# Kernel tuning notes

Measured on AMD Instinct MI355X. Metric: run time of the kernel, lower is better.

## Reference

```python
import jax, jax.numpy as jnp
import numpy as np

L = 3          # num_modification_layers
MOD_SCALE = 0.01


def setup_inputs() -> dict:
    key = jax.random.key(0)
    B, E = 8192, 1024
    ks = jax.random.split(key, 12)
    sg = 1.0 / np.sqrt(E)        # GRUCell / Linear(E,.) init bound
    sh = 1.0 / np.sqrt(E // 2)   # Linear(E//2, E) init bound
    u = lambda k, shape, s: jax.random.uniform(k, shape, jnp.float32, -s, s)
    return {
        "x":    jax.random.normal(ks[0], (B, E), jnp.float32),
        # GRUCell params (PyTorch layout: gates ordered r, z, n)
        "W_ih": u(ks[1], (L, 3 * E, E), sg),
        "W_hh": u(ks[2], (L, 3 * E, E), sg),
        "b_ih": u(ks[3], (L, 3 * E), sg),
        "b_hh": u(ks[4], (L, 3 * E), sg),
        # modification network: Linear(E, E//2) -> ReLU -> Linear(E//2, E) -> Tanh
        "W1":   u(ks[5], (L, E // 2, E), sg),
        "b1":   u(ks[6], (L, E // 2), sg),
        "W2":   u(ks[7], (L, E, E // 2), sh),
        "b2":   u(ks[8], (L, E), sh),
        # modification gate: Linear(E, 1) -> Sigmoid
        "Wg":   u(ks[9], (L, 1, E), sg),
        "bg":   u(ks[10], (L, 1), sg),
    }


def reference(x, W_ih, W_hh, b_ih, b_hh, W1, b1, W2, b2, Wg, bg):
    B, E = x.shape
    h_prev = jnp.zeros((B, E), x.dtype)  # hidden states reset to zeros
    cur = x
    for l in range(L):
        # modification network (small MLP) + scalar gate
        sig = jnp.tanh(jax.nn.relu(cur @ W1[l].T + b1[l]) @ W2[l].T + b2[l])  # (B, E)
        gate = jax.nn.sigmoid(cur @ Wg[l].T + bg[l])                           # (B, 1)
        cond = jnp.mean(gate) > 0.5
        # data-dependent self-modification: weight_ih += scale * mean(sig)[None,:]
        # (row-broadcast over the 3E gate rows), predicated on-device
        wih = jnp.where(cond,
                        W_ih[l] + MOD_SCALE * jnp.mean(sig, axis=0)[None, :],
                        W_ih[l])
        # GRUCell (PyTorch semantics)
        gi = cur @ wih.T + b_ih[l]            # (B, 3E)
        gh = h_prev @ W_hh[l].T + b_hh[l]     # (B, 3E) -- h_prev is zeros
        i_r, i_z, i_n = jnp.split(gi, 3, axis=1)
        h_r, h_z, h_n = jnp.split(gh, 3, axis=1)
        r = jax.nn.sigmoid(i_r + h_r)
        z = jax.nn.sigmoid(i_z + h_z)
        n = jnp.tanh(i_n + r * h_n)
        h = (1.0 - z) * n + z * h_prev
        cur = h + sig
    return cur
```

## Files before the change

kernel.cpp:

```cpp
#include <hip/hip_runtime.h>
#include <cstdint>
#include <cstddef>


#define BSZ 8192
#define ESZ 1024

typedef _Float16 f16x8 __attribute__((ext_vector_type(8)));
typedef float    f32x4 __attribute__((ext_vector_type(4)));
typedef unsigned short u16;
typedef u16 u16x4 __attribute__((ext_vector_type(4)));

__device__ __forceinline__ u16 f2h(float f) {
    _Float16 h = (_Float16)f;
    return __builtin_bit_cast(u16, h);
}

__device__ __forceinline__ void gload16(const void* g, void* l) {
    __builtin_amdgcn_global_load_lds((const __attribute__((address_space(1))) void*)g,
                                     (__attribute__((address_space(3))) void*)l,
                                     16, 0, 0);
}

__device__ __forceinline__ float sigmoidf_(float x) {
    return 1.f / (1.f + __expf(-x));
}
__device__ __forceinline__ float tanhf_(float x) {
    float cx = fminf(fmaxf(x, -15.f), 15.f);
    float e = __expf(2.f * cx);
    return (e - 1.f) / (e + 1.f);
}

__global__ void cvt_f16_kernel(const float* __restrict__ in, u16* __restrict__ out, int n4) {
    int i = blockIdx.x * 256 + threadIdx.x;
    if (i >= n4) return;
    f32x4 v = ((const f32x4*)in)[i];
    u16x4 o;
    o.x = f2h(v.x); o.y = f2h(v.y); o.z = f2h(v.z); o.w = f2h(v.w);
    ((u16x4*)out)[i] = o;
}

__global__ void gate_kernel(const float* __restrict__ cur, const float* __restrict__ Wg,
                            const float* __restrict__ bg, const float* __restrict__ colsum,
                            float* __restrict__ gsum, float* __restrict__ sdot) {
    const int wid = threadIdx.x >> 6, lane = threadIdx.x & 63;
    const int row = blockIdx.x * 4 + wid;
    const float* cr = cur + (size_t)row * ESZ;
    float pg = 0.f, pm = 0.f;
#pragma unroll
    for (int c = 0; c < 4; c++) {
        int idx = c * 256 + lane * 4;
        f32x4 cv = *(const f32x4*)(cr + idx);
        f32x4 wv = *(const f32x4*)(Wg + idx);
        f32x4 mv = *(const f32x4*)(colsum + idx);
        pg += cv.x * wv.x + cv.y * wv.y + cv.z * wv.z + cv.w * wv.w;
        pm += cv.x * mv.x + cv.y * mv.y + cv.z * mv.z + cv.w * mv.w;
    }
#pragma unroll
    for (int s = 32; s >= 1; s >>= 1) {
        pg += __shfl_xor(pg, s);
        pm += __shfl_xor(pm, s);
    }
    __shared__ float gp[4];
    if (lane == 0) {
        gp[wid] = sigmoidf_(pg + bg[0]);
        sdot[row] = pm * (0.01f / 8192.f);
    }
    __syncthreads();
    if (threadIdx.x == 0) atomicAdd(gsum, gp[0] + gp[1] + gp[2] + gp[3]);
}

template <int ACT>
__global__ void __launch_bounds__(256, 2) gemm_act_kernel(
    const u16* __restrict__ A, const u16* __restrict__ W,
    const float* __restrict__ bias, void* __restrict__ outp,
    float* __restrict__ colsum, int N, int K) {
    __shared__ u16 lA[128 * 64];
    __shared__ u16 lB[128 * 64];
    const int t = threadIdx.x;
    const int m0 = blockIdx.y * 128, n0 = blockIdx.x * 128;
    const int wid = t >> 6, lane = t & 63;
    const int waver = wid >> 1, wavec = wid & 1;
    const int lrow = lane & 15, lk = lane >> 4;

    f32x4 acc[4][4] = {};

    for (int k0 = 0; k0 < K; k0 += 64) {
        __syncthreads();
#pragma unroll
        for (int i = 0; i < 4; i++) {
            int eo = i * 2048 + t * 8;
            int r = eo >> 6, c = eo & 63;
            gload16(A + (size_t)(m0 + r) * K + k0 + c, &lA[eo]);
            gload16(W + (size_t)(n0 + r) * K + k0 + c, &lB[eo]);
        }
        __syncthreads();
#pragma unroll
        for (int kk = 0; kk < 2; kk++) {
            f16x8 af[4], bf[4];
#pragma unroll
            for (int m = 0; m < 4; m++)
                af[m] = *(const f16x8*)&lA[(waver * 64 + m * 16 + lrow) * 64 + kk * 32 + lk * 8];
#pragma unroll
            for (int n = 0; n < 4; n++)
                bf[n] = *(const f16x8*)&lB[(wavec * 64 + n * 16 + lrow) * 64 + kk * 32 + lk * 8];
#pragma unroll
            for (int m = 0; m < 4; m++)
#pragma unroll
                for (int n = 0; n < 4; n++)
                    acc[m][n] = __builtin_amdgcn_mfma_f32_16x16x32_f16(af[m], bf[n], acc[m][n], 0, 0, 0);
        }
    }

#pragma unroll
    for (int n = 0; n < 4; n++) {
        int c = n0 + wavec * 64 + n * 16 + lrow;
        float bv = bias[c];
        float cs = 0.f;
#pragma unroll
        for (int m = 0; m < 4; m++) {
            int rbase = m0 + waver * 64 + m * 16 + lk * 4;
#pragma unroll
            for (int j = 0; j < 4; j++) {
                float v = acc[m][n][j] + bv;
                if (ACT == 0) {
                    v = v > 0.f ? v : 0.f;
                    ((u16*)outp)[(size_t)(rbase + j) * N + c] = f2h(v);
                } else {
                    float tv = tanhf_(v);
                    ((float*)outp)[(size_t)(rbase + j) * N + c] = tv;
                    cs += tv;
                }
            }
        }
        if (ACT == 1) {
            cs += __shfl_xor(cs, 16);
            cs += __shfl_xor(cs, 32);
            if (lane < 16) atomicAdd(&colsum[c], cs);
        }
    }
}

__global__ void __launch_bounds__(256, 2) gemm_gru_kernel(
    const u16* __restrict__ Ab, const u16* __restrict__ Wb,
    const float* __restrict__ bih, const float* __restrict__ bhh,
    const float* __restrict__ sig, const float* __restrict__ sdot,
    const float* __restrict__ gsum, float* __restrict__ curf_out,
    u16* __restrict__ curb_out) {
    __shared__ u16 lA[128 * 64];
    __shared__ u16 lB[3][64 * 64];
    const int t = threadIdx.x;
    const int m0 = blockIdx.y * 128, c0 = blockIdx.x * 64;
    const int wid = t >> 6, lane = t & 63;
    const int waver = wid >> 1, wavec = wid & 1;
    const int lrow = lane & 15, lk = lane >> 4;
    const int K = ESZ, E = ESZ;

    f32x4 acc[4][6] = {};

    for (int k0 = 0; k0 < K; k0 += 64) {
        __syncthreads();
#pragma unroll
        for (int i = 0; i < 4; i++) {
            int eo = i * 2048 + t * 8;
            int r = eo >> 6, c = eo & 63;
            gload16(Ab + (size_t)(m0 + r) * K + k0 + c, &lA[eo]);
        }
#pragma unroll
        for (int g = 0; g < 3; g++)
#pragma unroll
            for (int i = 0; i < 2; i++) {
                int eo = i * 2048 + t * 8;
                int r = eo >> 6, c = eo & 63;
                gload16(Wb + (size_t)(g * 1024 + c0 + r) * K + k0 + c, &lB[g][eo]);
            }
        __syncthreads();
#pragma unroll
        for (int kk = 0; kk < 2; kk++) {
            f16x8 af[4];
#pragma unroll
            for (int m = 0; m < 4; m++)
                af[m] = *(const f16x8*)&lA[(waver * 64 + m * 16 + lrow) * 64 + kk * 32 + lk * 8];
#pragma unroll
            for (int g = 0; g < 3; g++) {
#pragma unroll
                for (int n = 0; n < 2; n++) {
                    f16x8 bf = *(const f16x8*)&lB[g][(wavec * 32 + n * 16 + lrow) * 64 + kk * 32 + lk * 8];
#pragma unroll
                    for (int m = 0; m < 4; m++)
                        acc[m][g * 2 + n] =
                            __builtin_amdgcn_mfma_f32_16x16x32_f16(af[m], bf, acc[m][g * 2 + n], 0, 0, 0);
                }
            }
        }
    }

    const bool cond = (*gsum) > 4096.f;
#pragma unroll
    for (int m = 0; m < 4; m++) {
        int rbase = m0 + waver * 64 + m * 16 + lk * 4;
        float corr[4];
#pragma unroll
        for (int j = 0; j < 4; j++) corr[j] = cond ? sdot[rbase + j] : 0.f;
#pragma unroll
        for (int n = 0; n < 2; n++) {
            int c = c0 + wavec * 32 + n * 16 + lrow;
            float br = bih[c], bz = bih[E + c], bn = bih[2 * E + c];
            float hr = bhh[c], hz = bhh[E + c], hn = bhh[2 * E + c];
#pragma unroll
            for (int j = 0; j < 4; j++) {
                float ir = acc[m][0 + n][j] + br + corr[j];
                float iz = acc[m][2 + n][j] + bz + corr[j];
                float inn = acc[m][4 + n][j] + bn + corr[j];
                float r = sigmoidf_(ir + hr);
                float z = sigmoidf_(iz + hz);
                float nn = tanhf_(inn + r * hn);
                float h = (1.f - z) * nn;
                float o = h + sig[(size_t)(rbase + j) * E + c];
                curf_out[(size_t)(rbase + j) * E + c] = o;
                if (curb_out) curb_out[(size_t)(rbase + j) * E + c] = f2h(o);
            }
        }
    }
}

extern "C" void kernel_launch(void* const* d_in, const int* in_sizes, int n_in,
                              void* d_out, int out_size, void* d_ws, size_t ws_size,
                              hipStream_t stream) {
    const float* x   = (const float*)d_in[0];
    const float* Wih = (const float*)d_in[1];
    const float* bih = (const float*)d_in[3];
    const float* bhh = (const float*)d_in[4];
    const float* W1  = (const float*)d_in[5];
    const float* b1  = (const float*)d_in[6];
    const float* W2  = (const float*)d_in[7];
    const float* b2  = (const float*)d_in[8];
    const float* Wg  = (const float*)d_in[9];
    const float* bg  = (const float*)d_in[10];
    float* out = (float*)d_out;

    char* w = (char*)d_ws;
    u16* Wihb  = (u16*)w;  w += (size_t)3 * 3072 * 1024 * 2;
    u16* W1b   = (u16*)w;  w += (size_t)3 * 512 * 1024 * 2;
    u16* W2b   = (u16*)w;  w += (size_t)3 * 1024 * 512 * 2;
    u16* curbA = (u16*)w;  w += (size_t)BSZ * ESZ * 2;
    u16* curbB = (u16*)w;  w += (size_t)BSZ * ESZ * 2;
    u16* Amat  = (u16*)w;  w += (size_t)BSZ * 512 * 2;
    float* sigb   = (float*)w;  w += (size_t)BSZ * ESZ * 4;
    float* colsum = (float*)w;  w += 4096;
    float* gsum   = (float*)w;  w += 256;
    float* sdot   = (float*)w;  w += (size_t)BSZ * 4;

    {
        int n4 = 3 * 3072 * 1024 / 4;
        cvt_f16_kernel<<<dim3((n4 + 255) / 256), 256, 0, stream>>>(Wih, Wihb, n4);
        n4 = 3 * 512 * 1024 / 4;
        cvt_f16_kernel<<<dim3((n4 + 255) / 256), 256, 0, stream>>>(W1, W1b, n4);
        n4 = 3 * 1024 * 512 / 4;
        cvt_f16_kernel<<<dim3((n4 + 255) / 256), 256, 0, stream>>>(W2, W2b, n4);
        n4 = BSZ * ESZ / 4;
        cvt_f16_kernel<<<dim3((n4 + 255) / 256), 256, 0, stream>>>(x, curbA, n4);
    }

    u16* cin = curbA;
    u16* cout = curbB;
    for (int l = 0; l < 3; l++) {
        hipMemsetAsync(colsum, 0, 4096 + 4, stream);
        gemm_act_kernel<0><<<dim3(512 / 128, BSZ / 128), 256, 0, stream>>>(
            cin, W1b + (size_t)l * 512 * 1024, b1 + l * 512, Amat, nullptr, 512, 1024);
        gemm_act_kernel<1><<<dim3(1024 / 128, BSZ / 128), 256, 0, stream>>>(
            Amat, W2b + (size_t)l * 1024 * 512, b2 + l * 1024, sigb, colsum, 1024, 512);
        gate_kernel<<<dim3(BSZ / 4), 256, 0, stream>>>(
            l == 0 ? x : out, Wg + l * 1024, bg + l, colsum, gsum, sdot);
        gemm_gru_kernel<<<dim3(ESZ / 64, BSZ / 128), 256, 0, stream>>>(
            cin, Wihb + (size_t)l * 3072 * 1024, bih + l * 3072, bhh + l * 3072,
            sigb, sdot, gsum, out, (l < 2) ? cout : nullptr);
        u16* tmp = cin; cin = cout; cout = tmp;
    }
}
```

Baseline: 635.6 us.

## Swizzle LDS tiles, store sig as fp16, fuse converts, remap GRU blocks per XCD

```diff
diff --git a/kernel.cpp b/kernel.cpp
--- a/kernel.cpp
+++ b/kernel.cpp
@@ -15,6 +15,9 @@
     _Float16 h = (_Float16)f;
     return __builtin_bit_cast(u16, h);
 }
+__device__ __forceinline__ float h2f(u16 h) {
+    return (float)__builtin_bit_cast(_Float16, h);
+}
 
 __device__ __forceinline__ void gload16(const void* g, void* l) {
     __builtin_amdgcn_global_load_lds((const __attribute__((address_space(1))) void*)g,
@@ -22,6 +25,10 @@
                                      16, 0, 0);
 }
 
+__device__ __forceinline__ int swzi(int row, int chunk) {
+    return (row << 6) + (((chunk ^ row) & 7) << 3);
+}
+
 __device__ __forceinline__ float sigmoidf_(float x) {
     return 1.f / (1.f + __expf(-x));
 }
@@ -31,30 +38,50 @@
     return (e - 1.f) / (e + 1.f);
 }
 
-__global__ void cvt_f16_kernel(const float* __restrict__ in, u16* __restrict__ out, int n4) {
+#define N4_WIH (3 * 3072 * 1024 / 4)
+#define N4_W1  (3 * 512 * 1024 / 4)
+#define N4_W2  (3 * 1024 * 512 / 4)
+#define N4_X   (BSZ * ESZ / 4)
+
+__global__ void cvt_all_kernel(const float* __restrict__ Wih, const float* __restrict__ W1,
+                               const float* __restrict__ W2, const float* __restrict__ x,
+                               u16* __restrict__ oWih, u16* __restrict__ oW1,
+                               u16* __restrict__ oW2, u16* __restrict__ ox) {
     int i = blockIdx.x * 256 + threadIdx.x;
-    if (i >= n4) return;
+    const float* in;
+    u16* out;
+    if (i < N4_WIH) { in = Wih; out = oWih; }
+    else if (i < N4_WIH + N4_W1) { i -= N4_WIH; in = W1; out = oW1; }
+    else if (i < N4_WIH + N4_W1 + N4_W2) { i -= N4_WIH + N4_W1; in = W2; out = oW2; }
+    else { i -= N4_WIH + N4_W1 + N4_W2; if (i >= N4_X) return; in = x; out = ox; }
     f32x4 v = ((const f32x4*)in)[i];
     u16x4 o;
     o.x = f2h(v.x); o.y = f2h(v.y); o.z = f2h(v.z); o.w = f2h(v.w);
     ((u16x4*)out)[i] = o;
 }
 
-__global__ void gate_kernel(const float* __restrict__ cur, const float* __restrict__ Wg,
+__global__ void gate_kernel(const u16* __restrict__ cur, const float* __restrict__ Wg,
                             const float* __restrict__ bg, const float* __restrict__ colsum,
                             float* __restrict__ gsum, float* __restrict__ sdot) {
     const int wid = threadIdx.x >> 6, lane = threadIdx.x & 63;
     const int row = blockIdx.x * 4 + wid;
-    const float* cr = cur + (size_t)row * ESZ;
+    const u16* cr = cur + (size_t)row * ESZ;
     float pg = 0.f, pm = 0.f;
 #pragma unroll
-    for (int c = 0; c < 4; c++) {
-        int idx = c * 256 + lane * 4;
-        f32x4 cv = *(const f32x4*)(cr + idx);
-        f32x4 wv = *(const f32x4*)(Wg + idx);
-        f32x4 mv = *(const f32x4*)(colsum + idx);
-        pg += cv.x * wv.x + cv.y * wv.y + cv.z * wv.z + cv.w * wv.w;
-        pm += cv.x * mv.x + cv.y * mv.y + cv.z * mv.z + cv.w * mv.w;
+    for (int h = 0; h < 2; h++) {
+        int base = lane * 16 + h * 8;
+        f16x8 cv = *(const f16x8*)(cr + base);
+#pragma unroll
+        for (int q = 0; q < 2; q++) {
+            f32x4 wv = *(const f32x4*)(Wg + base + q * 4);
+            f32x4 mv = *(const f32x4*)(colsum + base + q * 4);
+#pragma unroll
+            for (int e = 0; e < 4; e++) {
+                float c = (float)cv[q * 4 + e];
+                pg += c * wv[e];
+                pm += c * mv[e];
+            }
+        }
     }
 #pragma unroll
     for (int s = 32; s >= 1; s >>= 1) {
@@ -73,7 +100,7 @@
 template <int ACT>
 __global__ void __launch_bounds__(256, 2) gemm_act_kernel(
     const u16* __restrict__ A, const u16* __restrict__ W,
-    const float* __restrict__ bias, void* __restrict__ outp,
+    const float* __restrict__ bias, u16* __restrict__ outp,
     float* __restrict__ colsum, int N, int K) {
     __shared__ u16 lA[128 * 64];
     __shared__ u16 lB[128 * 64];
@@ -90,9 +117,10 @@
 #pragma unroll
         for (int i = 0; i < 4; i++) {
             int eo = i * 2048 + t * 8;
-            int r = eo >> 6, c = eo & 63;
-            gload16(A + (size_t)(m0 + r) * K + k0 + c, &lA[eo]);
-            gload16(W + (size_t)(n0 + r) * K + k0 + c, &lB[eo]);
+            int r = eo >> 6;
+            int gc = (((eo >> 3) ^ r) & 7) << 3;
+            gload16(A + (size_t)(m0 + r) * K + k0 + gc, &lA[eo]);
+            gload16(W + (size_t)(n0 + r) * K + k0 + gc, &lB[eo]);
         }
         __syncthreads();
 #pragma unroll
@@ -100,10 +128,10 @@
             f16x8 af[4], bf[4];
 #pragma unroll
             for (int m = 0; m < 4; m++)
-                af[m] = *(const f16x8*)&lA[(waver * 64 + m * 16 + lrow) * 64 + kk * 32 + lk * 8];
+                af[m] = *(const f16x8*)&lA[swzi(waver * 64 + m * 16 + lrow, kk * 4 + lk)];
 #pragma unroll
             for (int n = 0; n < 4; n++)
-                bf[n] = *(const f16x8*)&lB[(wavec * 64 + n * 16 + lrow) * 64 + kk * 32 + lk * 8];
+                bf[n] = *(const f16x8*)&lB[swzi(wavec * 64 + n * 16 + lrow, kk * 4 + lk)];
 #pragma unroll
             for (int m = 0; m < 4; m++)
 #pragma unroll
@@ -125,10 +153,10 @@
                 float v = acc[m][n][j] + bv;
                 if (ACT == 0) {
                     v = v > 0.f ? v : 0.f;
-                    ((u16*)outp)[(size_t)(rbase + j) * N + c] = f2h(v);
+                    outp[(size_t)(rbase + j) * N + c] = f2h(v);
                 } else {
                     float tv = tanhf_(v);
-                    ((float*)outp)[(size_t)(rbase + j) * N + c] = tv;
+                    outp[(size_t)(rbase + j) * N + c] = f2h(tv);
                     cs += tv;
                 }
             }
@@ -144,13 +172,15 @@
 __global__ void __launch_bounds__(256, 2) gemm_gru_kernel(
     const u16* __restrict__ Ab, const u16* __restrict__ Wb,
     const float* __restrict__ bih, const float* __restrict__ bhh,
-    const float* __restrict__ sig, const float* __restrict__ sdot,
+    const u16* __restrict__ sig, const float* __restrict__ sdot,
     const float* __restrict__ gsum, float* __restrict__ curf_out,
     u16* __restrict__ curb_out) {
     __shared__ u16 lA[128 * 64];
     __shared__ u16 lB[3][64 * 64];
     const int t = threadIdx.x;
-    const int m0 = blockIdx.y * 128, c0 = blockIdx.x * 64;
+    const int hw = blockIdx.y * 16 + blockIdx.x;
+    const int xcd = hw & 7, idx = hw >> 3;
+    const int m0 = (idx >> 1) * 128, c0 = ((xcd << 1) | (idx & 1)) * 64;
     const int wid = t >> 6, lane = t & 63;
     const int waver = wid >> 1, wavec = wid & 1;
     const int lrow = lane & 15, lk = lane >> 4;
@@ -163,16 +193,18 @@
 #pragma unroll
         for (int i = 0; i < 4; i++) {
             int eo = i * 2048 + t * 8;
-            int r = eo >> 6, c = eo & 63;
-            gload16(Ab + (size_t)(m0 + r) * K + k0 + c, &lA[eo]);
+            int r = eo >> 6;
+            int gc = (((eo >> 3) ^ r) & 7) << 3;
+            gload16(Ab + (size_t)(m0 + r) * K + k0 + gc, &lA[eo]);
         }
 #pragma unroll
         for (int g = 0; g < 3; g++)
 #pragma unroll
             for (int i = 0; i < 2; i++) {
                 int eo = i * 2048 + t * 8;
-                int r = eo >> 6, c = eo & 63;
-                gload16(Wb + (size_t)(g * 1024 + c0 + r) * K + k0 + c, &lB[g][eo]);
+                int r = eo >> 6;
+                int gc = (((eo >> 3) ^ r) & 7) << 3;
+                gload16(Wb + (size_t)(g * 1024 + c0 + r) * K + k0 + gc, &lB[g][eo]);
             }
         __syncthreads();
 #pragma unroll
@@ -180,12 +212,12 @@
             f16x8 af[4];
 #pragma unroll
             for (int m = 0; m < 4; m++)
-                af[m] = *(const f16x8*)&lA[(waver * 64 + m * 16 + lrow) * 64 + kk * 32 + lk * 8];
+                af[m] = *(const f16x8*)&lA[swzi(waver * 64 + m * 16 + lrow, kk * 4 + lk)];
 #pragma unroll
             for (int g = 0; g < 3; g++) {
 #pragma unroll
                 for (int n = 0; n < 2; n++) {
-                    f16x8 bf = *(const f16x8*)&lB[g][(wavec * 32 + n * 16 + lrow) * 64 + kk * 32 + lk * 8];
+                    f16x8 bf = *(const f16x8*)&lB[g][swzi(wavec * 32 + n * 16 + lrow, kk * 4 + lk)];
 #pragma unroll
                     for (int m = 0; m < 4; m++)
                         acc[m][g * 2 + n] =
@@ -216,8 +248,8 @@
                 float z = sigmoidf_(iz + hz);
                 float nn = tanhf_(inn + r * hn);
                 float h = (1.f - z) * nn;
-                float o = h + sig[(size_t)(rbase + j) * E + c];
-                curf_out[(size_t)(rbase + j) * E + c] = o;
+                float o = h + h2f(sig[(size_t)(rbase + j) * E + c]);
+                if (curf_out) curf_out[(size_t)(rbase + j) * E + c] = o;
                 if (curb_out) curb_out[(size_t)(rbase + j) * E + c] = f2h(o);
             }
         }
@@ -246,20 +278,15 @@
     u16* curbA = (u16*)w;  w += (size_t)BSZ * ESZ * 2;
     u16* curbB = (u16*)w;  w += (size_t)BSZ * ESZ * 2;
     u16* Amat  = (u16*)w;  w += (size_t)BSZ * 512 * 2;
-    float* sigb   = (float*)w;  w += (size_t)BSZ * ESZ * 4;
+    u16* sigb  = (u16*)w;  w += (size_t)BSZ * ESZ * 2;
     float* colsum = (float*)w;  w += 4096;
     float* gsum   = (float*)w;  w += 256;
     float* sdot   = (float*)w;  w += (size_t)BSZ * 4;
 
     {
-        int n4 = 3 * 3072 * 1024 / 4;
-        cvt_f16_kernel<<<dim3((n4 + 255) / 256), 256, 0, stream>>>(Wih, Wihb, n4);
-        n4 = 3 * 512 * 1024 / 4;
-        cvt_f16_kernel<<<dim3((n4 + 255) / 256), 256, 0, stream>>>(W1, W1b, n4);
-        n4 = 3 * 1024 * 512 / 4;
-        cvt_f16_kernel<<<dim3((n4 + 255) / 256), 256, 0, stream>>>(W2, W2b, n4);
-        n4 = BSZ * ESZ / 4;
-        cvt_f16_kernel<<<dim3((n4 + 255) / 256), 256, 0, stream>>>(x, curbA, n4);
+        int n4 = N4_WIH + N4_W1 + N4_W2 + N4_X;
+        cvt_all_kernel<<<dim3((n4 + 255) / 256), 256, 0, stream>>>(
+            Wih, W1, W2, x, Wihb, W1b, W2b, curbA);
     }
 
     u16* cin = curbA;
@@ -271,10 +298,10 @@
         gemm_act_kernel<1><<<dim3(1024 / 128, BSZ / 128), 256, 0, stream>>>(
             Amat, W2b + (size_t)l * 1024 * 512, b2 + l * 1024, sigb, colsum, 1024, 512);
         gate_kernel<<<dim3(BSZ / 4), 256, 0, stream>>>(
-            l == 0 ? x : out, Wg + l * 1024, bg + l, colsum, gsum, sdot);
-        gemm_gru_kernel<<<dim3(ESZ / 64, BSZ / 128), 256, 0, stream>>>(
+            cin, Wg + l * 1024, bg + l, colsum, gsum, sdot);
+        gemm_gru_kernel<<<dim3(16, BSZ / 128), 256, 0, stream>>>(
             cin, Wihb + (size_t)l * 3072 * 1024, bih + l * 3072, bhh + l * 3072,
-            sigb, sdot, gsum, out, (l < 2) ? cout : nullptr);
+            sigb, sdot, gsum, (l == 2) ? out : nullptr, (l < 2) ? cout : nullptr);
         u16* tmp = cin; cin = cout; cout = tmp;
     }
 }
```

After: 590.5 us. 1.08x faster.
